# Optimization experiments

Measured on AMD Instinct MI355X. Metric: run time of the kernel, lower is better.

The kernel has to match this reference:

```python
import jax, jax.numpy as jnp
import numpy as np

N = 33554432  # batch of discriminator scores

def setup_inputs() -> dict:
    key = jax.random.key(0)
    k1, k2 = jax.random.split(key)
    D_label = jax.random.normal(k1, (N,), dtype=jnp.float32)
    # targets in {-1, +1} as in the original GAN hinge-loss convention
    t01 = jax.random.randint(k2, (N,), 0, 2, dtype=jnp.int32)
    target_label = 2 * t01 - 1
    return {"D_label": D_label, "target_label": target_label}

def reference(D_label, target_label):
    # Hinge GAN loss: for t==+1 add min(0, D-1); for t==-1 add min(0, -1-D);
    # other targets contribute 0. Then divide by batch size.
    zero = jnp.float32(0)
    pos = jnp.minimum(zero, D_label - 1.0)   # target == +1
    neg = jnp.minimum(zero, -1.0 - D_label)  # target == -1
    contrib = jnp.where(target_label == 1, pos,
              jnp.where(target_label == -1, neg, zero))
    g_loss = jnp.sum(contrib) / jnp.float32(D_label.shape[0])
    return g_loss.reshape(1)  # original returns a shape-(1,) tensor
```

## Files before the change

### kernel.cpp

```cpp
#include <hip/hip_runtime.h>


__global__ __launch_bounds__(256) void ganloss_kernel(
    const float* __restrict__ D, const int* __restrict__ T,
    float* __restrict__ out, int n4, float inv_n) {
  const float4* __restrict__ D4 = reinterpret_cast<const float4*>(D);
  const int4* __restrict__ T4 = reinterpret_cast<const int4*>(T);

  int tid = blockIdx.x * blockDim.x + threadIdx.x;
  int stride = gridDim.x * blockDim.x;

  float acc = 0.0f;
  for (int i = tid; i < n4; i += stride) {
    float4 d = D4[i];
    int4 t = T4[i];
    float tf0 = (float)t.x, tf1 = (float)t.y, tf2 = (float)t.z, tf3 = (float)t.w;
    float c0 = (t.x * t.x == 1) ? fminf(0.0f, tf0 * (d.x - tf0)) : 0.0f;
    float c1 = (t.y * t.y == 1) ? fminf(0.0f, tf1 * (d.y - tf1)) : 0.0f;
    float c2 = (t.z * t.z == 1) ? fminf(0.0f, tf2 * (d.z - tf2)) : 0.0f;
    float c3 = (t.w * t.w == 1) ? fminf(0.0f, tf3 * (d.w - tf3)) : 0.0f;
    acc += (c0 + c1) + (c2 + c3);
  }

  #pragma unroll
  for (int off = 32; off > 0; off >>= 1)
    acc += __shfl_down(acc, off, 64);

  __shared__ float wsum[4];
  int lane = threadIdx.x & 63;
  int wid = threadIdx.x >> 6;
  if (lane == 0) wsum[wid] = acc;
  __syncthreads();

  if (threadIdx.x == 0) {
    float s = (wsum[0] + wsum[1]) + (wsum[2] + wsum[3]);
    atomicAdd(out, s * inv_n);
  }
}

extern "C" void kernel_launch(void* const* d_in, const int* in_sizes, int n_in,
                              void* d_out, int out_size, void* d_ws, size_t ws_size,
                              hipStream_t stream) {
  const float* D = (const float*)d_in[0];
  const int* T = (const int*)d_in[1];
  float* out = (float*)d_out;
  int n = in_sizes[0];
  int n4 = n >> 2;
  float inv_n = 1.0f / (float)n;

  hipMemsetAsync(d_out, 0, out_size * sizeof(float), stream);

  const int block = 256;
  int grid = 2048;
  ganloss_kernel<<<grid, block, 0, stream>>>(D, T, out, n4, inv_n);
}
```

Before: 283.6 us.

## Replace memset and atomic reduction with two-pass partials reduction

Each block now writes its partial sum to workspace, and a second single-block kernel sums the 2048 partials and scales by 1/n. This drops the hipMemsetAsync launch and the 2048 same-address atomics in exchange for one extra small kernel launch. The per-element math also becomes fma(t, d, -1), which equals t*(d-t) for t in {-1,+1} and saves an instruction in a kernel that is bound by memory bandwidth.

Measured after the change: 274.9 us. 1.03x faster.

```diff
diff --git a/kernel.cpp b/kernel.cpp
--- a/kernel.cpp
+++ b/kernel.cpp
@@ -1,9 +1,9 @@
 #include <hip/hip_runtime.h>
 
 
-__global__ __launch_bounds__(256) void ganloss_kernel(
+__global__ __launch_bounds__(256) void ganloss_partial(
     const float* __restrict__ D, const int* __restrict__ T,
-    float* __restrict__ out, int n4, float inv_n) {
+    float* __restrict__ partials, int n4) {
   const float4* __restrict__ D4 = reinterpret_cast<const float4*>(D);
   const int4* __restrict__ T4 = reinterpret_cast<const int4*>(T);
 
@@ -14,11 +14,10 @@
   for (int i = tid; i < n4; i += stride) {
     float4 d = D4[i];
     int4 t = T4[i];
-    float tf0 = (float)t.x, tf1 = (float)t.y, tf2 = (float)t.z, tf3 = (float)t.w;
-    float c0 = (t.x * t.x == 1) ? fminf(0.0f, tf0 * (d.x - tf0)) : 0.0f;
-    float c1 = (t.y * t.y == 1) ? fminf(0.0f, tf1 * (d.y - tf1)) : 0.0f;
-    float c2 = (t.z * t.z == 1) ? fminf(0.0f, tf2 * (d.z - tf2)) : 0.0f;
-    float c3 = (t.w * t.w == 1) ? fminf(0.0f, tf3 * (d.w - tf3)) : 0.0f;
+    float c0 = (t.x * t.x == 1) ? fminf(0.0f, __fmaf_rn((float)t.x, d.x, -1.0f)) : 0.0f;
+    float c1 = (t.y * t.y == 1) ? fminf(0.0f, __fmaf_rn((float)t.y, d.y, -1.0f)) : 0.0f;
+    float c2 = (t.z * t.z == 1) ? fminf(0.0f, __fmaf_rn((float)t.z, d.z, -1.0f)) : 0.0f;
+    float c3 = (t.w * t.w == 1) ? fminf(0.0f, __fmaf_rn((float)t.w, d.w, -1.0f)) : 0.0f;
     acc += (c0 + c1) + (c2 + c3);
   }
 
@@ -32,10 +31,29 @@
   if (lane == 0) wsum[wid] = acc;
   __syncthreads();
 
-  if (threadIdx.x == 0) {
-    float s = (wsum[0] + wsum[1]) + (wsum[2] + wsum[3]);
-    atomicAdd(out, s * inv_n);
-  }
+  if (threadIdx.x == 0)
+    partials[blockIdx.x] = (wsum[0] + wsum[1]) + (wsum[2] + wsum[3]);
+}
+
+__global__ __launch_bounds__(256) void ganloss_final(
+    const float* __restrict__ partials, float* __restrict__ out,
+    int nparts, float inv_n) {
+  float acc = 0.0f;
+  for (int i = threadIdx.x; i < nparts; i += 256)
+    acc += partials[i];
+
+  #pragma unroll
+  for (int off = 32; off > 0; off >>= 1)
+    acc += __shfl_down(acc, off, 64);
+
+  __shared__ float wsum[4];
+  int lane = threadIdx.x & 63;
+  int wid = threadIdx.x >> 6;
+  if (lane == 0) wsum[wid] = acc;
+  __syncthreads();
+
+  if (threadIdx.x == 0)
+    out[0] = ((wsum[0] + wsum[1]) + (wsum[2] + wsum[3])) * inv_n;
 }
 
 extern "C" void kernel_launch(void* const* d_in, const int* in_sizes, int n_in,
@@ -44,13 +62,14 @@
   const float* D = (const float*)d_in[0];
   const int* T = (const int*)d_in[1];
   float* out = (float*)d_out;
+  float* partials = (float*)d_ws;
   int n = in_sizes[0];
   int n4 = n >> 2;
   float inv_n = 1.0f / (float)n;
 
-  hipMemsetAsync(d_out, 0, out_size * sizeof(float), stream);
+  const int block = 256;
+  const int grid = 2048;
 
-  const int block = 256;
-  int grid = 2048;
-  ganloss_kernel<<<grid, block, 0, stream>>>(D, T, out, n4, inv_n);
+  ganloss_partial<<<grid, block, 0, stream>>>(D, T, partials, n4);
+  ganloss_final<<<1, block, 0, stream>>>(partials, out, grid, inv_n);
 }
```
